# Kernel tuning notes

Measured on AMD Instinct MI355X. Metric: run time of the kernel, lower is better.

Reference implementation:

```python
import jax, jax.numpy as jnp
import numpy as np

B, S, H, NH, SPAN = 1, 2048, 768, 12, 512
D = H // NH
EPS = 1e-7
SCALE_FACTOR = 3  # 1 + len([c2p, p2c]) per DeBERTa


def setup_inputs() -> dict:
    key = jax.random.key(0)
    ks = jax.random.split(key, 10)
    r = lambda i, shape, s=0.02: jax.random.normal(ks[i], shape, jnp.float32) * s
    return dict(
        hidden_states=jax.random.normal(ks[0], (B, S, H), jnp.float32),
        attention_mask=jnp.ones((B, S), jnp.int32),
        Wq=r(1, (H, H)), bq=jnp.zeros((H,), jnp.float32),
        Wk=r(2, (H, H)), bk=jnp.zeros((H,), jnp.float32),
        Wv=r(3, (H, H)), bv=jnp.zeros((H,), jnp.float32),
        rel_embeddings=r(4, (2 * SPAN, H), 1.0),
        Wpk=r(5, (H, H)),
        Wpq=r(6, (H, H)), bpq=jnp.zeros((H,), jnp.float32),
        Wo=r(7, (H, H)), bo=jnp.zeros((H,), jnp.float32),
        ln_gamma=jnp.ones((H,), jnp.float32),
        ln_beta=jnp.zeros((H,), jnp.float32),
    )


def _heads(x):
    # [B,S,H] -> [B,NH,S,D]
    return x.reshape(B, S, NH, D).transpose(0, 2, 1, 3)


def reference(hidden_states, attention_mask, Wq, bq, Wk, bk, Wv, bv,
              rel_embeddings, Wpk, Wpq, bpq, Wo, bo, ln_gamma, ln_beta):
    q = _heads(hidden_states @ Wq + bq)
    k = _heads(hidden_states @ Wk + bk)
    v = _heads(hidden_states @ Wv + bv)
    scale = 1.0 / jnp.sqrt(jnp.asarray(D * SCALE_FACTOR, jnp.float32))

    # content-to-content
    scores = jnp.einsum('bhid,bhjd->bhij', q, k) * scale

    # relative positions: rel[i,j] = i - j
    ids = jnp.arange(S)
    rel = ids[:, None] - ids[None, :]                       # [S,S]

    pos_k = (rel_embeddings @ Wpk).reshape(2 * SPAN, NH, D)        # [2L,h,d]
    pos_q = (rel_embeddings @ Wpq + bpq).reshape(2 * SPAN, NH, D)  # [2L,h,d]

    # content-to-position: gather over clamped relative index
    c2p = jnp.einsum('bhid,lhd->bhil', q, pos_k) * scale    # [B,h,S,2L]
    c2p_idx = jnp.clip(rel + SPAN, 0, 2 * SPAN - 1)         # [S,S]
    c2p_att = c2p[:, :, ids[:, None], c2p_idx]              # [B,h,S,S]

    # position-to-content: gather then transpose (DeBERTa)
    p2c = jnp.einsum('bhjd,lhd->bhjl', k, pos_q) * scale    # [B,h,S,2L]
    p2c_idx = jnp.clip(-rel + SPAN, 0, 2 * SPAN - 1)        # [S,S]
    p2c_att = jnp.swapaxes(p2c[:, :, ids[:, None], p2c_idx], -1, -2)

    scores = scores + c2p_att + p2c_att

    mask4 = (attention_mask[:, None, None, :] * attention_mask[:, None, :, None]).astype(bool)
    scores = jnp.where(mask4, scores, jnp.finfo(scores.dtype).min)
    probs = jax.nn.softmax(scores, axis=-1)

    ctx = jnp.einsum('bhij,bhjd->bhid', probs, v).transpose(0, 2, 1, 3).reshape(B, S, H)

    # BertSelfOutput: dense + (dropout=identity) + residual + LayerNorm
    out = ctx @ Wo + bo + hidden_states
    mu = out.mean(-1, keepdims=True)
    var = out.var(-1, keepdims=True)
    return (out - mu) / jnp.sqrt(var + EPS) * ln_gamma + ln_beta
```

## Files before the change

### kernel.cpp

```cpp
#include <hip/hip_runtime.h>
#include <hip/hip_bf16.h>


typedef short v8s __attribute__((ext_vector_type(8)));
typedef short v4s __attribute__((ext_vector_type(4)));
typedef float v4f __attribute__((ext_vector_type(4)));

__device__ __forceinline__ float b2f(unsigned short u) {
    union { unsigned int i; float f; } v; v.i = ((unsigned int)u) << 16; return v.f;
}
__device__ __forceinline__ unsigned short f2b(float f) {
    union { float f; unsigned int i; } v; v.f = f;
    unsigned int x = v.i;
    return (unsigned short)((x + 0x7FFFu + ((x >> 16) & 1u)) >> 16);
}

#define SEQ 2048
#define HD  768
#define NH_ 12
#define DH  64

__global__ void cvt_kernel(const float* __restrict__ hs, const float* __restrict__ rel,
                           const float* __restrict__ bq, const float* __restrict__ bk,
                           const float* __restrict__ bv, const float* __restrict__ bpq,
                           unsigned short* __restrict__ Xb, unsigned short* __restrict__ Rb,
                           float* __restrict__ bias3, float* __restrict__ bias2) {
    long i = (long)blockIdx.x * 256 + threadIdx.x;
    const long n1 = (long)SEQ * HD;
    const long n2 = 1024l * HD;
    if (i < n1) Xb[i] = f2b(hs[i]);
    else if (i < n1 + n2) Rb[i - n1] = f2b(rel[i - n1]);
    else {
        int j = (int)(i - n1 - n2);
        if (j < 768)        bias3[j] = bq[j];
        else if (j < 1536)  bias3[j] = bk[j - 768];
        else if (j < 2304)  bias3[j] = bv[j - 1536];
        else if (j < 3072)  bias2[j - 2304] = 0.0f;
        else if (j < 3840)  bias2[j - 2304] = bpq[j - 3072];
    }
}

struct WtArgs { const float* src[6]; unsigned short* dst[6]; };
__global__ void wtrans_kernel(WtArgs args) {
    __shared__ float tile[32][33];
    const int z = blockIdx.z;
    const float* Sp = args.src[z];
    unsigned short* Dp = args.dst[z];
    const int bx = blockIdx.x * 32, by = blockIdx.y * 32;
    const int tx = threadIdx.x, ty = threadIdx.y;
#pragma unroll
    for (int r = 0; r < 32; r += 8) tile[ty + r][tx] = Sp[(by + ty + r) * HD + bx + tx];
    __syncthreads();
#pragma unroll
    for (int r = 0; r < 32; r += 8) Dp[(bx + ty + r) * HD + by + tx] = f2b(tile[tx][ty + r]);
}

__global__ void vtrans_kernel(const unsigned short* __restrict__ src,
                              unsigned short* __restrict__ dst) {
    __shared__ unsigned short tile[32][33];
    const int bx = blockIdx.x * 32, by = blockIdx.y * 32;
    const int tx = threadIdx.x, ty = threadIdx.y;
#pragma unroll
    for (int r = 0; r < 32; r += 8) tile[ty + r][tx] = src[(long)(by + ty + r) * HD + bx + tx];
    __syncthreads();
#pragma unroll
    for (int r = 0; r < 32; r += 8) dst[(long)(bx + ty + r) * SEQ + by + tx] = tile[tx][ty + r];
}

template <int BIAS, int RESID, int OUTF32>
__global__ __launch_bounds__(256) void gemm_bt(
    const unsigned short* __restrict__ A, int lda, long aBatch,
    const unsigned short* __restrict__ Bt, int ldb, long bBatch,
    void* __restrict__ Cv, int ldc, long cBatch,
    const float* __restrict__ bias, long biasBatch,
    const float* __restrict__ resid, int K) {
    __shared__ unsigned short As[128 * 72];
    __shared__ unsigned short Bs[128 * 72];
    const int z = blockIdx.z;
    const unsigned short* Ab = A + (long)z * aBatch;
    const unsigned short* Bb = Bt + (long)z * bBatch;
    const int m0 = blockIdx.y * 128, n0 = blockIdx.x * 128;
    const int t = threadIdx.x;
    const int wave = t >> 6, lane = t & 63, quad = lane >> 4, l16 = lane & 15;
    const int wm = (wave >> 1) * 64, wn = (wave & 1) * 64;
    v4f acc[4][4];
    const v4f z4 = {0.f, 0.f, 0.f, 0.f};
#pragma unroll
    for (int i = 0; i < 4; i++)
#pragma unroll
        for (int j = 0; j < 4; j++) acc[i][j] = z4;

    const int srow = t >> 1, scol = (t & 1) * 32;
    const unsigned short* ga = Ab + (long)(m0 + srow) * lda + scol;
    const unsigned short* gb = Bb + (long)(n0 + srow) * ldb + scol;
    unsigned short* wa = &As[srow * 72 + scol];
    unsigned short* wb = &Bs[srow * 72 + scol];

    for (int k0 = 0; k0 < K; k0 += 64) {
        __syncthreads();
        v8s a0 = *(const v8s*)(ga + k0);
        v8s a1 = *(const v8s*)(ga + k0 + 8);
        v8s a2 = *(const v8s*)(ga + k0 + 16);
        v8s a3 = *(const v8s*)(ga + k0 + 24);
        v8s b0 = *(const v8s*)(gb + k0);
        v8s b1 = *(const v8s*)(gb + k0 + 8);
        v8s b2 = *(const v8s*)(gb + k0 + 16);
        v8s b3 = *(const v8s*)(gb + k0 + 24);
        *(v8s*)(wa) = a0; *(v8s*)(wa + 8) = a1; *(v8s*)(wa + 16) = a2; *(v8s*)(wa + 24) = a3;
        *(v8s*)(wb) = b0; *(v8s*)(wb + 8) = b1; *(v8s*)(wb + 16) = b2; *(v8s*)(wb + 24) = b3;
        __syncthreads();
#pragma unroll
        for (int ks = 0; ks < 2; ks++) {
            v8s af[4], bf[4];
#pragma unroll
            for (int mt = 0; mt < 4; mt++)
                af[mt] = *(const v8s*)&As[(wm + 16 * mt + l16) * 72 + ks * 32 + quad * 8];
#pragma unroll
            for (int nt = 0; nt < 4; nt++)
                bf[nt] = *(const v8s*)&Bs[(wn + 16 * nt + l16) * 72 + ks * 32 + quad * 8];
#pragma unroll
            for (int mt = 0; mt < 4; mt++)
#pragma unroll
                for (int nt = 0; nt < 4; nt++)
                    acc[mt][nt] = __builtin_amdgcn_mfma_f32_16x16x32_bf16(af[mt], bf[nt], acc[mt][nt], 0, 0, 0);
        }
    }
    float* Cf = (float*)Cv;
    unsigned short* Ch = (unsigned short*)Cv;
    const long cb = (long)z * cBatch;
#pragma unroll
    for (int mt = 0; mt < 4; mt++) {
#pragma unroll
        for (int nt = 0; nt < 4; nt++) {
            const int gn = n0 + wn + 16 * nt + l16;
            float bv_ = 0.0f;
            if (BIAS) bv_ = bias[(long)z * biasBatch + gn];
#pragma unroll
            for (int r = 0; r < 4; r++) {
                const int gm = m0 + wm + 16 * mt + quad * 4 + r;
                float v = acc[mt][nt][r];
                if (BIAS) v += bv_;
                if (RESID) v += resid[(long)gm * ldc + gn];
                if (OUTF32) Cf[cb + (long)gm * ldc + gn] = v;
                else        Ch[cb + (long)gm * ldc + gn] = f2b(v);
            }
        }
    }
}

__device__ __forceinline__ void stage_window(const unsigned short* __restrict__ row,
                                             int D0, v8s& w0, v8s& w1) {
    if (D0 <= 0) {
        unsigned short v = row[0];
#pragma unroll
        for (int u = 0; u < 8; u++) { w0[u] = (short)v; w1[u] = (short)v; }
    } else if (D0 - 15 >= 1023) {
        unsigned short v = row[1023];
#pragma unroll
        for (int u = 0; u < 8; u++) { w0[u] = (short)v; w1[u] = (short)v; }
    } else if (D0 <= 1023 && D0 - 15 >= 0) {
        v8s x = *(const v8s*)(row + D0 - 7);
        v8s y = *(const v8s*)(row + D0 - 15);
#pragma unroll
        for (int u = 0; u < 8; u++) { w0[u] = x[7 - u]; w1[u] = y[7 - u]; }
    } else {
#pragma unroll
        for (int u = 0; u < 16; u++) {
            int d = D0 - u; d = d < 0 ? 0 : (d > 1023 ? 1023 : d);
            short v = (short)row[d];
            if (u < 8) w0[u] = v; else w1[u - 8] = v;
        }
    }
}

__global__ __launch_bounds__(256, 3) void flash_kernel(
    const unsigned short* __restrict__ qb, const unsigned short* __restrict__ kb,
    const unsigned short* __restrict__ vT, const unsigned short* __restrict__ c2p,
    const unsigned short* __restrict__ p2c, float* __restrict__ opart,
    float* __restrict__ mlpart) {
    __shared__ unsigned short Kl[64 * 72];
    __shared__ unsigned short Vl[64 * 72];
    __shared__ unsigned short Pl[4][16 * 72];
    __shared__ unsigned short Cw[64 * 72];
    __shared__ unsigned short Pw[64 * 72];
    const int h = blockIdx.y;
    const int i0 = blockIdx.x * 64;
    const int jc = blockIdx.z;
    const int jbase = jc * 1024;
    const int t = threadIdx.x;
    const int wave = t >> 6, lane = t & 63, quad = lane >> 4, l16 = lane & 15;
    const float scale = 0.07216878364870322f;

    v8s qf[2];
    {
        const int irow = i0 + wave * 16 + l16;
        const unsigned short* qp = qb + (long)irow * HD + h * DH + quad * 8;
        qf[0] = *(const v8s*)qp;
        qf[1] = *(const v8s*)(qp + 32);
    }
    float m_run[4] = {-1e30f, -1e30f, -1e30f, -1e30f};
    float l_run[4] = {0.f, 0.f, 0.f, 0.f};
    v4f o_acc[4];
    const v4f z4 = {0.f, 0.f, 0.f, 0.f};
#pragma unroll
    for (int nt = 0; nt < 4; nt++) o_acc[nt] = z4;

    const int srow = t >> 2, scoff = (t & 3) * 16;
    const unsigned short* kbase = kb + (long)srow * HD + h * DH + scoff;
    const unsigned short* vbase = vT + (long)(h * DH + srow) * SEQ + scoff + jbase;
    unsigned short* wk = &Kl[srow * 72 + scoff];
    unsigned short* wv = &Vl[srow * 72 + scoff];
    const unsigned short* c2prow = c2p + ((long)h * SEQ + i0 + srow) * 1024;
    const unsigned short* p2cb = p2c + (long)h * SEQ * 1024;

    v8s k0v, k1v, v0v, v1v, cw0, cw1, pw0, pw1;
    auto load_tile = [&](int j0) {
        k0v = *(const v8s*)(kbase + (long)(jbase + j0) * HD);
        k1v = *(const v8s*)(kbase + (long)(jbase + j0) * HD + 8);
        v0v = *(const v8s*)(vbase + j0);
        v1v = *(const v8s*)(vbase + j0 + 8);
        stage_window(c2prow, (i0 + srow) - (jbase + j0) - scoff + 512, cw0, cw1);
        stage_window(p2cb + (long)(jbase + j0 + srow) * 1024,
                     (jbase + j0 + srow) - i0 - scoff + 512, pw0, pw1);
    };
    load_tile(0);

    for (int tt = 0; tt < 16; tt++) {
        __syncthreads();
        *(v8s*)wk = k0v; *(v8s*)(wk + 8) = k1v;
        *(v8s*)wv = v0v; *(v8s*)(wv + 8) = v1v;
        *(v8s*)&Cw[srow * 72 + scoff] = cw0; *(v8s*)&Cw[srow * 72 + scoff + 8] = cw1;
        *(v8s*)&Pw[srow * 72 + scoff] = pw0; *(v8s*)&Pw[srow * 72 + scoff + 8] = pw1;
        if (tt + 1 < 16) load_tile((tt + 1) * 64);
        __syncthreads();

        v4f s[4];
#pragma unroll
        for (int nt = 0; nt < 4; nt++) s[nt] = z4;
#pragma unroll
        for (int ks = 0; ks < 2; ks++) {
#pragma unroll
            for (int nt = 0; nt < 4; nt++) {
                v8s bf = *(const v8s*)&Kl[(16 * nt + l16) * 72 + ks * 32 + quad * 8];
                s[nt] = __builtin_amdgcn_mfma_f32_16x16x32_bf16(qf[ks], bf, s[nt], 0, 0, 0);
            }
        }
        float sm[4][4];
#pragma unroll
        for (int nt = 0; nt < 4; nt++) {
            v4s p4 = *(const v4s*)&Pw[(nt * 16 + l16) * 72 + wave * 16 + quad * 4];
#pragma unroll
            for (int r = 0; r < 4; r++) {
                float c2pv = b2f(Cw[(wave * 16 + quad * 4 + r) * 72 + nt * 16 + l16]);
                float p2cv = b2f((unsigned short)p4[r]);
                sm[nt][r] = (s[nt][r] + c2pv + p2cv) * scale;
            }
        }
#pragma unroll
        for (int r = 0; r < 4; r++) {
            float mx = fmaxf(fmaxf(sm[0][r], sm[1][r]), fmaxf(sm[2][r], sm[3][r]));
#pragma unroll
            for (int off = 1; off < 16; off <<= 1) mx = fmaxf(mx, __shfl_xor(mx, off));
            float mnew = fmaxf(m_run[r], mx);
            float alpha = __expf(m_run[r] - mnew);
            m_run[r] = mnew;
            float rs = 0.f;
#pragma unroll
            for (int nt = 0; nt < 4; nt++) {
                float p = __expf(sm[nt][r] - mnew);
                sm[nt][r] = p;
                rs += p;
            }
#pragma unroll
            for (int off = 1; off < 16; off <<= 1) rs += __shfl_xor(rs, off);
            l_run[r] = l_run[r] * alpha + rs;
#pragma unroll
            for (int nt = 0; nt < 4; nt++) o_acc[nt][r] *= alpha;
        }
#pragma unroll
        for (int nt = 0; nt < 4; nt++)
#pragma unroll
            for (int r = 0; r < 4; r++)
                Pl[wave][(quad * 4 + r) * 72 + nt * 16 + l16] = f2b(sm[nt][r]);
        __syncthreads();
#pragma unroll
        for (int ks = 0; ks < 2; ks++) {
            v8s pf = *(const v8s*)&Pl[wave][l16 * 72 + ks * 32 + quad * 8];
#pragma unroll
            for (int nt = 0; nt < 4; nt++) {
                v8s vf = *(const v8s*)&Vl[(16 * nt + l16) * 72 + ks * 32 + quad * 8];
                o_acc[nt] = __builtin_amdgcn_mfma_f32_16x16x32_bf16(pf, vf, o_acc[nt], 0, 0, 0);
            }
        }
    }
    float* op = opart + (long)jc * SEQ * HD;
#pragma unroll
    for (int nt = 0; nt < 4; nt++) {
        const int d = nt * 16 + l16;
#pragma unroll
        for (int r = 0; r < 4; r++) {
            const int i = i0 + wave * 16 + quad * 4 + r;
            op[(long)i * HD + h * DH + d] = o_acc[nt][r];
        }
    }
    if (l16 == 0) {
#pragma unroll
        for (int r = 0; r < 4; r++) {
            const int i = i0 + wave * 16 + quad * 4 + r;
            float* ml = mlpart + (((long)jc * NH_ + h) * SEQ + i) * 2;
            ml[0] = m_run[r];
            ml[1] = l_run[r];
        }
    }
}

__global__ __launch_bounds__(256) void combine_kernel(const float* __restrict__ opart,
                                                      const float* __restrict__ mlpart,
                                                      unsigned short* __restrict__ ctx) {
    const long idx = (long)blockIdx.x * 256 + threadIdx.x;
    const int i = (int)(idx / HD);
    const int hd = (int)(idx % HD);
    const int h = hd >> 6;
    const float* ml0 = mlpart + (((long)0 * NH_ + h) * SEQ + i) * 2;
    const float* ml1 = mlpart + (((long)1 * NH_ + h) * SEQ + i) * 2;
    float m0 = ml0[0], l0 = ml0[1], m1 = ml1[0], l1 = ml1[1];
    float mM = fmaxf(m0, m1);
    float w0 = __expf(m0 - mM), w1 = __expf(m1 - mM);
    float num = w0 * opart[idx] + w1 * opart[(long)SEQ * HD + idx];
    float den = w0 * l0 + w1 * l1;
    ctx[idx] = f2b(num / den);
}

__global__ __launch_bounds__(256) void ln_kernel(const float* __restrict__ x,
                                                 const float* __restrict__ gamma,
                                                 const float* __restrict__ beta,
                                                 float* __restrict__ out) {
    const int row = blockIdx.x;
    const int t = threadIdx.x;
    const float* xr = x + (long)row * HD;
    float v0 = xr[t], v1 = xr[t + 256], v2 = xr[t + 512];
    float s = v0 + v1 + v2;
    float ss = v0 * v0 + v1 * v1 + v2 * v2;
#pragma unroll
    for (int off = 1; off < 64; off <<= 1) { s += __shfl_xor(s, off); ss += __shfl_xor(ss, off); }
    __shared__ float red[8];
    const int wave = t >> 6;
    if ((t & 63) == 0) { red[wave] = s; red[wave + 4] = ss; }
    __syncthreads();
    float S = red[0] + red[1] + red[2] + red[3];
    float SS = red[4] + red[5] + red[6] + red[7];
    const float inv = 1.0f / 768.0f;
    float mu = S * inv;
    float var = SS * inv - mu * mu;
    float rstd = rsqrtf(var + 1e-7f);
    float* orow = out + (long)row * HD;
    orow[t]       = (v0 - mu) * rstd * gamma[t]       + beta[t];
    orow[t + 256] = (v1 - mu) * rstd * gamma[t + 256] + beta[t + 256];
    orow[t + 512] = (v2 - mu) * rstd * gamma[t + 512] + beta[t + 512];
}

extern "C" void kernel_launch(void* const* d_in, const int* in_sizes, int n_in,
                              void* d_out, int out_size, void* d_ws, size_t ws_size,
                              hipStream_t stream) {
    const float* hidden = (const float*)d_in[0];
    const float* Wq  = (const float*)d_in[2];
    const float* bq  = (const float*)d_in[3];
    const float* Wk  = (const float*)d_in[4];
    const float* bk  = (const float*)d_in[5];
    const float* Wv  = (const float*)d_in[6];
    const float* bv  = (const float*)d_in[7];
    const float* rel = (const float*)d_in[8];
    const float* Wpk = (const float*)d_in[9];
    const float* Wpq = (const float*)d_in[10];
    const float* bpq = (const float*)d_in[11];
    const float* Wo  = (const float*)d_in[12];
    const float* bo  = (const float*)d_in[13];
    const float* gamma = (const float*)d_in[14];
    const float* beta  = (const float*)d_in[15];

    char* ws = (char*)d_ws;
    size_t off = 0;
    auto alloc = [&](size_t bytes) -> char* { char* p = ws + off; off += bytes; return p; };
    unsigned short* Xb   = (unsigned short*)alloc(2048ul * 768 * 2);
    unsigned short* Rb   = (unsigned short*)alloc(1024ul * 768 * 2);
    unsigned short* W3T  = (unsigned short*)alloc(3ul * 768 * 768 * 2);
    unsigned short* WoT  = (unsigned short*)alloc(768ul * 768 * 2);
    unsigned short* Wp2T = (unsigned short*)alloc(2ul * 768 * 768 * 2);
    float*          bias3 = (float*)alloc(2304 * 4);
    float*          bias2 = (float*)alloc(1536 * 4);
    unsigned short* qkv  = (unsigned short*)alloc(3ul * 2048 * 768 * 2);
    unsigned short* vTs  = (unsigned short*)alloc(768ul * 2048 * 2);
    unsigned short* pos2 = (unsigned short*)alloc(2ul * 1024 * 768 * 2);
    unsigned short* c2p  = (unsigned short*)alloc(12ul * 2048 * 1024 * 2);
    unsigned short* p2c  = (unsigned short*)alloc(12ul * 2048 * 1024 * 2);
    unsigned short* ctx  = (unsigned short*)alloc(2048ul * 768 * 2);
    float*          out_pre = (float*)alloc(2048ul * 768 * 4);
    float*          opart   = (float*)alloc(2ul * 2048 * 768 * 4);
    float*          mlpart  = (float*)alloc(2ul * 12 * 2048 * 2 * 4);
    (void)ws_size;

    cvt_kernel<<<9231, 256, 0, stream>>>(hidden, rel, bq, bk, bv, bpq, Xb, Rb, bias3, bias2);
    WtArgs wa;
    wa.src[0] = Wq;  wa.dst[0] = W3T;
    wa.src[1] = Wk;  wa.dst[1] = W3T + 768 * 768;
    wa.src[2] = Wv;  wa.dst[2] = W3T + 2 * 768 * 768;
    wa.src[3] = Wo;  wa.dst[3] = WoT;
    wa.src[4] = Wpk; wa.dst[4] = Wp2T;
    wa.src[5] = Wpq; wa.dst[5] = Wp2T + 768 * 768;
    wtrans_kernel<<<dim3(24, 24, 6), dim3(32, 8), 0, stream>>>(wa);

    gemm_bt<1, 0, 0><<<dim3(6, 16, 3), 256, 0, stream>>>(
        Xb, 768, 0, W3T, 768, 768l * 768, qkv, 768, 2048l * 768, bias3, 768, nullptr, 768);
    gemm_bt<1, 0, 0><<<dim3(6, 8, 2), 256, 0, stream>>>(
        Rb, 768, 0, Wp2T, 768, 768l * 768, pos2, 768, 1024l * 768, bias2, 768, nullptr, 768);
    vtrans_kernel<<<dim3(24, 64), dim3(32, 8), 0, stream>>>(qkv + 2ul * 2048 * 768, vTs);
    gemm_bt<0, 0, 0><<<dim3(8, 16, 12), 256, 0, stream>>>(
        qkv, 768, 64, pos2, 768, 64, c2p, 1024, 2048l * 1024, nullptr, 0, nullptr, 64);
    gemm_bt<0, 0, 0><<<dim3(8, 16, 12), 256, 0, stream>>>(
        qkv + 2048ul * 768, 768, 64, pos2 + 1024ul * 768, 768, 64, p2c, 1024, 2048l * 1024,
        nullptr, 0, nullptr, 64);
    flash_kernel<<<dim3(32, 12, 2), 256, 0, stream>>>(qkv, qkv + 2048ul * 768, vTs, c2p, p2c,
                                                      opart, mlpart);
    combine_kernel<<<6144, 256, 0, stream>>>(opart, mlpart, ctx);
    gemm_bt<1, 1, 1><<<dim3(6, 16, 1), 256, 0, stream>>>(
        ctx, 768, 0, WoT, 768, 0, out_pre, 768, 0, bo, 0, hidden, 768);
    ln_kernel<<<2048, 256, 0, stream>>>(out_pre, gamma, beta, (float*)d_out);
}
```

Measured before the change: 269.6 us.

## Fuse c2p/p2c position GEMMs into flash attention kernel, drop score buffers

Stops materialising the full c2p and p2c score tables (12x2048x1024 bf16 each) through two separate GEMM launches. The flash kernel now computes the needed 64-wide relative-position windows on the fly with MFMA against pos_k/pos_q, keeping them in small LDS rings indexed by the diagonal offset. K and V tiles are read straight from global memory instead of being staged through LDS. This removes large HBM writes and reads and two launches, at the cost of extra MFMA work and uncoalesced, unprefetched global loads inside the attention loop.

```diff
diff --git a/kernel.cpp b/kernel.cpp
--- a/kernel.cpp
+++ b/kernel.cpp
@@ -3,7 +3,6 @@
 
 
 typedef short v8s __attribute__((ext_vector_type(8)));
-typedef short v4s __attribute__((ext_vector_type(4)));
 typedef float v4f __attribute__((ext_vector_type(4)));
 
 __device__ __forceinline__ float b2f(unsigned short u) {
@@ -148,111 +147,125 @@
     }
 }
 
-__device__ __forceinline__ void stage_window(const unsigned short* __restrict__ row,
-                                             int D0, v8s& w0, v8s& w1) {
-    if (D0 <= 0) {
-        unsigned short v = row[0];
-#pragma unroll
-        for (int u = 0; u < 8; u++) { w0[u] = (short)v; w1[u] = (short)v; }
-    } else if (D0 - 15 >= 1023) {
-        unsigned short v = row[1023];
-#pragma unroll
-        for (int u = 0; u < 8; u++) { w0[u] = (short)v; w1[u] = (short)v; }
-    } else if (D0 <= 1023 && D0 - 15 >= 0) {
-        v8s x = *(const v8s*)(row + D0 - 7);
-        v8s y = *(const v8s*)(row + D0 - 15);
-#pragma unroll
-        for (int u = 0; u < 8; u++) { w0[u] = x[7 - u]; w1[u] = y[7 - u]; }
-    } else {
-#pragma unroll
-        for (int u = 0; u < 16; u++) {
-            int d = D0 - u; d = d < 0 ? 0 : (d > 1023 ? 1023 : d);
-            short v = (short)row[d];
-            if (u < 8) w0[u] = v; else w1[u - 8] = v;
-        }
-    }
-}
-
 __global__ __launch_bounds__(256, 3) void flash_kernel(
     const unsigned short* __restrict__ qb, const unsigned short* __restrict__ kb,
-    const unsigned short* __restrict__ vT, const unsigned short* __restrict__ c2p,
-    const unsigned short* __restrict__ p2c, float* __restrict__ opart,
+    const unsigned short* __restrict__ vT, const unsigned short* __restrict__ posk,
+    const unsigned short* __restrict__ posq, float* __restrict__ opart,
     float* __restrict__ mlpart) {
-    __shared__ unsigned short Kl[64 * 72];
-    __shared__ unsigned short Vl[64 * 72];
+    __shared__ unsigned short Cring[4][2][16 * 68];
+    __shared__ unsigned short Pring[2][64 * 68];
     __shared__ unsigned short Pl[4][16 * 72];
-    __shared__ unsigned short Cw[64 * 72];
-    __shared__ unsigned short Pw[64 * 72];
     const int h = blockIdx.y;
     const int i0 = blockIdx.x * 64;
-    const int jc = blockIdx.z;
-    const int jbase = jc * 1024;
+    const int jbase = blockIdx.z * 1024;
     const int t = threadIdx.x;
     const int wave = t >> 6, lane = t & 63, quad = lane >> 4, l16 = lane & 15;
     const float scale = 0.07216878364870322f;
+    const v4f z4 = {0.f, 0.f, 0.f, 0.f};
+
+    const unsigned short* pkh = posk + h * DH;
+    const unsigned short* pqh = posq + h * DH;
+    const unsigned short* kbh = kb + h * DH;
+    const unsigned short* vth = vT + (long)h * DH * SEQ;
 
     v8s qf[2];
     {
-        const int irow = i0 + wave * 16 + l16;
-        const unsigned short* qp = qb + (long)irow * HD + h * DH + quad * 8;
+        const unsigned short* qp = qb + (long)(i0 + wave * 16 + l16) * HD + h * DH + quad * 8;
         qf[0] = *(const v8s*)qp;
         qf[1] = *(const v8s*)(qp + 32);
     }
+
     float m_run[4] = {-1e30f, -1e30f, -1e30f, -1e30f};
     float l_run[4] = {0.f, 0.f, 0.f, 0.f};
     v4f o_acc[4];
-    const v4f z4 = {0.f, 0.f, 0.f, 0.f};
 #pragma unroll
     for (int nt = 0; nt < 4; nt++) o_acc[nt] = z4;
 
-    const int srow = t >> 2, scoff = (t & 3) * 16;
-    const unsigned short* kbase = kb + (long)srow * HD + h * DH + scoff;
-    const unsigned short* vbase = vT + (long)(h * DH + srow) * SEQ + scoff + jbase;
-    unsigned short* wk = &Kl[srow * 72 + scoff];
-    unsigned short* wv = &Vl[srow * 72 + scoff];
-    const unsigned short* c2prow = c2p + ((long)h * SEQ + i0 + srow) * 1024;
-    const unsigned short* p2cb = p2c + (long)h * SEQ * 1024;
-
-    v8s k0v, k1v, v0v, v1v, cw0, cw1, pw0, pw1;
-    auto load_tile = [&](int j0) {
-        k0v = *(const v8s*)(kbase + (long)(jbase + j0) * HD);
-        k1v = *(const v8s*)(kbase + (long)(jbase + j0) * HD + 8);
-        v0v = *(const v8s*)(vbase + j0);
-        v1v = *(const v8s*)(vbase + j0 + 8);
-        stage_window(c2prow, (i0 + srow) - (jbase + j0) - scoff + 512, cw0, cw1);
-        stage_window(p2cb + (long)(jbase + j0 + srow) * 1024,
-                     (jbase + j0 + srow) - i0 - scoff + 512, pw0, pw1);
+    unsigned short* cw = &Cring[wave][0][0];
+
+    auto c2p_block = [&](int b) {
+        v4f c[4] = {z4, z4, z4, z4};
+        int rr[4];
+#pragma unroll
+        for (int nt = 0; nt < 4; nt++) {
+            int r = 64 * b + 16 * nt + l16;
+            rr[nt] = r < 0 ? 0 : (r > 1023 ? 1023 : r);
+        }
+#pragma unroll
+        for (int ks = 0; ks < 2; ks++)
+#pragma unroll
+            for (int nt = 0; nt < 4; nt++) {
+                v8s bf = *(const v8s*)(pkh + (long)rr[nt] * HD + ks * 32 + quad * 8);
+                c[nt] = __builtin_amdgcn_mfma_f32_16x16x32_bf16(qf[ks], bf, c[nt], 0, 0, 0);
+            }
+        unsigned short* dst = cw + (b & 1) * (16 * 68);
+#pragma unroll
+        for (int nt = 0; nt < 4; nt++)
+#pragma unroll
+            for (int r = 0; r < 4; r++)
+                dst[(quad * 4 + r) * 68 + 16 * nt + l16] = f2b(c[nt][r]);
     };
-    load_tile(0);
 
     for (int tt = 0; tt < 16; tt++) {
+        const int j0 = jbase + 64 * tt;
+        const int D = i0 - j0 + 512;
+        const int BLc = (D >> 6) - 1;
+        const int Bp = ((j0 - i0 + 512) >> 6) - 1;
+
         __syncthreads();
-        *(v8s*)wk = k0v; *(v8s*)(wk + 8) = k1v;
-        *(v8s*)wv = v0v; *(v8s*)(wv + 8) = v1v;
-        *(v8s*)&Cw[srow * 72 + scoff] = cw0; *(v8s*)&Cw[srow * 72 + scoff + 8] = cw1;
-        *(v8s*)&Pw[srow * 72 + scoff] = pw0; *(v8s*)&Pw[srow * 72 + scoff + 8] = pw1;
-        if (tt + 1 < 16) load_tile((tt + 1) * 64);
+        if (tt == 0) c2p_block(BLc + 1);
+        c2p_block(BLc);
+        {
+            v8s af[2];
+#pragma unroll
+            for (int ks = 0; ks < 2; ks++)
+                af[ks] = *(const v8s*)(kbh + (long)(j0 + wave * 16 + l16) * HD + ks * 32 + quad * 8);
+#pragma unroll
+            for (int sel = 0; sel < 2; sel++) {
+                const int b = Bp + sel;
+                v4f p[4] = {z4, z4, z4, z4};
+                int rr[4];
+#pragma unroll
+                for (int nt = 0; nt < 4; nt++) {
+                    int r = 64 * b + 16 * nt + l16;
+                    rr[nt] = r < 0 ? 0 : (r > 1023 ? 1023 : r);
+                }
+#pragma unroll
+                for (int ks = 0; ks < 2; ks++)
+#pragma unroll
+                    for (int nt = 0; nt < 4; nt++) {
+                        v8s bf = *(const v8s*)(pqh + (long)rr[nt] * HD + ks * 32 + quad * 8);
+                        p[nt] = __builtin_amdgcn_mfma_f32_16x16x32_bf16(af[ks], bf, p[nt], 0, 0, 0);
+                    }
+#pragma unroll
+                for (int nt = 0; nt < 4; nt++)
+#pragma unroll
+                    for (int r = 0; r < 4; r++)
+                        Pring[sel][(wave * 16 + quad * 4 + r) * 68 + 16 * nt + l16] = f2b(p[nt][r]);
+            }
+        }
+        v4f s[4] = {z4, z4, z4, z4};
+#pragma unroll
+        for (int ks = 0; ks < 2; ks++)
+#pragma unroll
+            for (int nt = 0; nt < 4; nt++) {
+                v8s bf = *(const v8s*)(kbh + (long)(j0 + 16 * nt + l16) * HD + ks * 32 + quad * 8);
+                s[nt] = __builtin_amdgcn_mfma_f32_16x16x32_bf16(qf[ks], bf, s[nt], 0, 0, 0);
+            }
         __syncthreads();
 
-        v4f s[4];
-#pragma unroll
-        for (int nt = 0; nt < 4; nt++) s[nt] = z4;
-#pragma unroll
-        for (int ks = 0; ks < 2; ks++) {
-#pragma unroll
-            for (int nt = 0; nt < 4; nt++) {
-                v8s bf = *(const v8s*)&Kl[(16 * nt + l16) * 72 + ks * 32 + quad * 8];
-                s[nt] = __builtin_amdgcn_mfma_f32_16x16x32_bf16(qf[ks], bf, s[nt], 0, 0, 0);
-            }
-        }
         float sm[4][4];
 #pragma unroll
         for (int nt = 0; nt < 4; nt++) {
-            v4s p4 = *(const v4s*)&Pw[(nt * 16 + l16) * 72 + wave * 16 + quad * 4];
 #pragma unroll
             for (int r = 0; r < 4; r++) {
-                float c2pv = b2f(Cw[(wave * 16 + quad * 4 + r) * 72 + nt * 16 + l16]);
-                float p2cv = b2f((unsigned short)p4[r]);
+                const int il = wave * 16 + quad * 4 + r;
+                const int jl = nt * 16 + l16;
+                const int idx = 64 + il - jl;
+                float c2pv = b2f(cw[((BLc + (idx >> 6)) & 1) * (16 * 68) +
+                                    (quad * 4 + r) * 68 + (idx & 63)]);
+                const int idq = 128 - idx;
+                float p2cv = b2f(Pring[idq >> 6][jl * 68 + (idq & 63)]);
                 sm[nt][r] = (s[nt][r] + c2pv + p2cv) * scale;
             }
         }
@@ -288,11 +301,12 @@
             v8s pf = *(const v8s*)&Pl[wave][l16 * 72 + ks * 32 + quad * 8];
 #pragma unroll
             for (int nt = 0; nt < 4; nt++) {
-                v8s vf = *(const v8s*)&Vl[(16 * nt + l16) * 72 + ks * 32 + quad * 8];
+                v8s vf = *(const v8s*)(vth + (long)(16 * nt + l16) * SEQ + j0 + ks * 32 + quad * 8);
                 o_acc[nt] = __builtin_amdgcn_mfma_f32_16x16x32_bf16(pf, vf, o_acc[nt], 0, 0, 0);
             }
         }
     }
+    const int jc = blockIdx.z;
     float* op = opart + (long)jc * SEQ * HD;
 #pragma unroll
     for (int nt = 0; nt < 4; nt++) {
@@ -391,8 +405,6 @@
     unsigned short* qkv  = (unsigned short*)alloc(3ul * 2048 * 768 * 2);
     unsigned short* vTs  = (unsigned short*)alloc(768ul * 2048 * 2);
     unsigned short* pos2 = (unsigned short*)alloc(2ul * 1024 * 768 * 2);
-    unsigned short* c2p  = (unsigned short*)alloc(12ul * 2048 * 1024 * 2);
-    unsigned short* p2c  = (unsigned short*)alloc(12ul * 2048 * 1024 * 2);
     unsigned short* ctx  = (unsigned short*)alloc(2048ul * 768 * 2);
     float*          out_pre = (float*)alloc(2048ul * 768 * 4);
     float*          opart   = (float*)alloc(2ul * 2048 * 768 * 4);
@@ -414,13 +426,8 @@
     gemm_bt<1, 0, 0><<<dim3(6, 8, 2), 256, 0, stream>>>(
         Rb, 768, 0, Wp2T, 768, 768l * 768, pos2, 768, 1024l * 768, bias2, 768, nullptr, 768);
     vtrans_kernel<<<dim3(24, 64), dim3(32, 8), 0, stream>>>(qkv + 2ul * 2048 * 768, vTs);
-    gemm_bt<0, 0, 0><<<dim3(8, 16, 12), 256, 0, stream>>>(
-        qkv, 768, 64, pos2, 768, 64, c2p, 1024, 2048l * 1024, nullptr, 0, nullptr, 64);
-    gemm_bt<0, 0, 0><<<dim3(8, 16, 12), 256, 0, stream>>>(
-        qkv + 2048ul * 768, 768, 64, pos2 + 1024ul * 768, 768, 64, p2c, 1024, 2048l * 1024,
-        nullptr, 0, nullptr, 64);
-    flash_kernel<<<dim3(32, 12, 2), 256, 0, stream>>>(qkv, qkv + 2048ul * 768, vTs, c2p, p2c,
-                                                      opart, mlpart);
+    flash_kernel<<<dim3(32, 12, 2), 256, 0, stream>>>(qkv, qkv + 2048ul * 768, vTs,
+                                                      pos2, pos2 + 1024ul * 768, opart, mlpart);
     combine_kernel<<<6144, 256, 0, stream>>>(opart, mlpart, ctx);
     gemm_bt<1, 1, 1><<<dim3(6, 16, 1), 256, 0, stream>>>(
         ctx, 768, 0, WoT, 768, 0, out_pre, 768, 0, bo, 0, hidden, 768);
```

New measurement: 372.2 us. 1.38x slower.

## Merge prep and GEMM launches, shrink flash LDS to raise occupancy

Applied to the files above, without the earlier changes.

Folds the conversion and weight-transpose kernels into one launch, merges the QKV and positional GEMMs into one grid, and merges the c2p and p2c GEMMs into one grid, cutting the number of kernel launches and the idle gaps between them. In the flash kernel, the per-wave probability buffer now shares one LDS array with the c2p window, and the block barrier before the PV product is replaced by an LDS waitcnt. This lowers LDS use so the launch bound can ask for 4 blocks per CU instead of 3. The shared buffer relies on each wave touching only its own rows, and the strided prep loop adds some per-element overhead.

```diff
diff --git a/kernel.cpp b/kernel.cpp
--- a/kernel.cpp
+++ b/kernel.cpp
@@ -20,39 +20,44 @@
 #define NH_ 12
 #define DH  64
 
-__global__ void cvt_kernel(const float* __restrict__ hs, const float* __restrict__ rel,
-                           const float* __restrict__ bq, const float* __restrict__ bk,
-                           const float* __restrict__ bv, const float* __restrict__ bpq,
-                           unsigned short* __restrict__ Xb, unsigned short* __restrict__ Rb,
-                           float* __restrict__ bias3, float* __restrict__ bias2) {
-    long i = (long)blockIdx.x * 256 + threadIdx.x;
-    const long n1 = (long)SEQ * HD;
-    const long n2 = 1024l * HD;
-    if (i < n1) Xb[i] = f2b(hs[i]);
-    else if (i < n1 + n2) Rb[i - n1] = f2b(rel[i - n1]);
-    else {
-        int j = (int)(i - n1 - n2);
-        if (j < 768)        bias3[j] = bq[j];
-        else if (j < 1536)  bias3[j] = bk[j - 768];
-        else if (j < 2304)  bias3[j] = bv[j - 1536];
-        else if (j < 3072)  bias2[j - 2304] = 0.0f;
-        else if (j < 3840)  bias2[j - 2304] = bpq[j - 3072];
-    }
-}
-
 struct WtArgs { const float* src[6]; unsigned short* dst[6]; };
-__global__ void wtrans_kernel(WtArgs args) {
-    __shared__ float tile[32][33];
+__global__ void prep_kernel(WtArgs args, const float* __restrict__ hs,
+                            const float* __restrict__ rel,
+                            const float* __restrict__ bq, const float* __restrict__ bk,
+                            const float* __restrict__ bv, const float* __restrict__ bpq,
+                            unsigned short* __restrict__ Xb, unsigned short* __restrict__ Rb,
+                            float* __restrict__ bias3, float* __restrict__ bias2) {
     const int z = blockIdx.z;
-    const float* Sp = args.src[z];
-    unsigned short* Dp = args.dst[z];
-    const int bx = blockIdx.x * 32, by = blockIdx.y * 32;
     const int tx = threadIdx.x, ty = threadIdx.y;
-#pragma unroll
-    for (int r = 0; r < 32; r += 8) tile[ty + r][tx] = Sp[(by + ty + r) * HD + bx + tx];
-    __syncthreads();
-#pragma unroll
-    for (int r = 0; r < 32; r += 8) Dp[(bx + ty + r) * HD + by + tx] = f2b(tile[tx][ty + r]);
+    if (z < 6) {
+        __shared__ float tile[32][33];
+        const float* Sp = args.src[z];
+        unsigned short* Dp = args.dst[z];
+        const int bx = blockIdx.x * 32, by = blockIdx.y * 32;
+#pragma unroll
+        for (int r = 0; r < 32; r += 8) tile[ty + r][tx] = Sp[(by + ty + r) * HD + bx + tx];
+        __syncthreads();
+#pragma unroll
+        for (int r = 0; r < 32; r += 8) Dp[(bx + ty + r) * HD + by + tx] = f2b(tile[tx][ty + r]);
+    } else {
+        const long n1 = (long)SEQ * HD;
+        const long n2 = 1024l * HD;
+        const long N = n1 + n2 + 3840;
+        const long stride = 24l * 24 * 256;
+        long i = ((long)blockIdx.y * 24 + blockIdx.x) * 256 + ty * 32 + tx;
+        for (; i < N; i += stride) {
+            if (i < n1) Xb[i] = f2b(hs[i]);
+            else if (i < n1 + n2) Rb[i - n1] = f2b(rel[i - n1]);
+            else {
+                int j = (int)(i - n1 - n2);
+                if (j < 768)        bias3[j] = bq[j];
+                else if (j < 1536)  bias3[j] = bk[j - 768];
+                else if (j < 2304)  bias3[j] = bv[j - 1536];
+                else if (j < 3072)  bias2[j - 2304] = 0.0f;
+                else                bias2[j - 2304] = bpq[j - 3072];
+            }
+        }
+    }
 }
 
 __global__ void vtrans_kernel(const unsigned short* __restrict__ src,
@@ -68,18 +73,12 @@
 }
 
 template <int BIAS, int RESID, int OUTF32>
-__global__ __launch_bounds__(256) void gemm_bt(
-    const unsigned short* __restrict__ A, int lda, long aBatch,
-    const unsigned short* __restrict__ Bt, int ldb, long bBatch,
-    void* __restrict__ Cv, int ldc, long cBatch,
-    const float* __restrict__ bias, long biasBatch,
-    const float* __restrict__ resid, int K) {
-    __shared__ unsigned short As[128 * 72];
-    __shared__ unsigned short Bs[128 * 72];
-    const int z = blockIdx.z;
-    const unsigned short* Ab = A + (long)z * aBatch;
-    const unsigned short* Bb = Bt + (long)z * bBatch;
-    const int m0 = blockIdx.y * 128, n0 = blockIdx.x * 128;
+__device__ __forceinline__ void gemm_core(
+    const unsigned short* __restrict__ A, int lda,
+    const unsigned short* __restrict__ Bt, int ldb,
+    void* __restrict__ Cv, int ldc,
+    const float* __restrict__ bias, const float* __restrict__ resid,
+    int K, int m0, int n0, unsigned short* As, unsigned short* Bs) {
     const int t = threadIdx.x;
     const int wave = t >> 6, lane = t & 63, quad = lane >> 4, l16 = lane & 15;
     const int wm = (wave >> 1) * 64, wn = (wave & 1) * 64;
@@ -91,8 +90,8 @@
         for (int j = 0; j < 4; j++) acc[i][j] = z4;
 
     const int srow = t >> 1, scol = (t & 1) * 32;
-    const unsigned short* ga = Ab + (long)(m0 + srow) * lda + scol;
-    const unsigned short* gb = Bb + (long)(n0 + srow) * ldb + scol;
+    const unsigned short* ga = A + (long)(m0 + srow) * lda + scol;
+    const unsigned short* gb = Bt + (long)(n0 + srow) * ldb + scol;
     unsigned short* wa = &As[srow * 72 + scol];
     unsigned short* wb = &Bs[srow * 72 + scol];
 
@@ -127,25 +126,75 @@
     }
     float* Cf = (float*)Cv;
     unsigned short* Ch = (unsigned short*)Cv;
-    const long cb = (long)z * cBatch;
 #pragma unroll
     for (int mt = 0; mt < 4; mt++) {
 #pragma unroll
         for (int nt = 0; nt < 4; nt++) {
             const int gn = n0 + wn + 16 * nt + l16;
             float bv_ = 0.0f;
-            if (BIAS) bv_ = bias[(long)z * biasBatch + gn];
+            if (BIAS) bv_ = bias[gn];
 #pragma unroll
             for (int r = 0; r < 4; r++) {
                 const int gm = m0 + wm + 16 * mt + quad * 4 + r;
                 float v = acc[mt][nt][r];
                 if (BIAS) v += bv_;
                 if (RESID) v += resid[(long)gm * ldc + gn];
-                if (OUTF32) Cf[cb + (long)gm * ldc + gn] = v;
-                else        Ch[cb + (long)gm * ldc + gn] = f2b(v);
-            }
-        }
-    }
+                if (OUTF32) Cf[(long)gm * ldc + gn] = v;
+                else        Ch[(long)gm * ldc + gn] = f2b(v);
+            }
+        }
+    }
+}
+
+__global__ __launch_bounds__(256) void gemm_qkvpos(
+    const unsigned short* __restrict__ Xb, const unsigned short* __restrict__ Rb,
+    const unsigned short* __restrict__ W3T, const unsigned short* __restrict__ Wp2T,
+    const float* __restrict__ bias3, const float* __restrict__ bias2,
+    unsigned short* __restrict__ qkv, unsigned short* __restrict__ pos2) {
+    __shared__ unsigned short As[128 * 72];
+    __shared__ unsigned short Bs[128 * 72];
+    const int z = blockIdx.z;
+    if (z < 3) {
+        gemm_core<1, 0, 0>(Xb, 768, W3T + (long)z * 768 * 768, 768,
+                           qkv + (long)z * 2048 * 768, 768, bias3 + z * 768, nullptr,
+                           768, blockIdx.y * 128, blockIdx.x * 128, As, Bs);
+    } else {
+        if (blockIdx.y >= 8) return;
+        const int w = z - 3;
+        gemm_core<1, 0, 0>(Rb, 768, Wp2T + (long)w * 768 * 768, 768,
+                           pos2 + (long)w * 1024 * 768, 768, bias2 + w * 768, nullptr,
+                           768, blockIdx.y * 128, blockIdx.x * 128, As, Bs);
+    }
+}
+
+__global__ __launch_bounds__(256) void gemm_band(
+    const unsigned short* __restrict__ qkv, const unsigned short* __restrict__ pos2,
+    unsigned short* __restrict__ c2p, unsigned short* __restrict__ p2c) {
+    __shared__ unsigned short As[128 * 72];
+    __shared__ unsigned short Bs[128 * 72];
+    const int z = blockIdx.z;
+    const unsigned short* A;
+    const unsigned short* B;
+    unsigned short* C;
+    if (z < 12) {
+        A = qkv + z * 64; B = pos2 + z * 64; C = c2p + (long)z * 2048 * 1024;
+    } else {
+        const int h = z - 12;
+        A = qkv + 2048l * 768 + h * 64; B = pos2 + 1024l * 768 + h * 64;
+        C = p2c + (long)h * 2048 * 1024;
+    }
+    gemm_core<0, 0, 0>(A, 768, B, 768, C, 1024, nullptr, nullptr,
+                       64, blockIdx.y * 128, blockIdx.x * 128, As, Bs);
+}
+
+__global__ __launch_bounds__(256) void gemm_out(
+    const unsigned short* __restrict__ ctx, const unsigned short* __restrict__ WoT,
+    const float* __restrict__ bo, const float* __restrict__ hidden,
+    float* __restrict__ out_pre) {
+    __shared__ unsigned short As[128 * 72];
+    __shared__ unsigned short Bs[128 * 72];
+    gemm_core<1, 1, 1>(ctx, 768, WoT, 768, out_pre, 768, bo, hidden,
+                       768, blockIdx.y * 128, blockIdx.x * 128, As, Bs);
 }
 
 __device__ __forceinline__ void stage_window(const unsigned short* __restrict__ row,
@@ -173,16 +222,15 @@
     }
 }
 
-__global__ __launch_bounds__(256, 3) void flash_kernel(
+__global__ __launch_bounds__(256, 4) void flash_kernel(
     const unsigned short* __restrict__ qb, const unsigned short* __restrict__ kb,
     const unsigned short* __restrict__ vT, const unsigned short* __restrict__ c2p,
     const unsigned short* __restrict__ p2c, float* __restrict__ opart,
     float* __restrict__ mlpart) {
     __shared__ unsigned short Kl[64 * 72];
     __shared__ unsigned short Vl[64 * 72];
-    __shared__ unsigned short Pl[4][16 * 72];
-    __shared__ unsigned short Cw[64 * 72];
     __shared__ unsigned short Pw[64 * 72];
+    __shared__ unsigned short CwPl[64 * 72];
     const int h = blockIdx.y;
     const int i0 = blockIdx.x * 64;
     const int jc = blockIdx.z;
@@ -190,18 +238,17 @@
     const int t = threadIdx.x;
     const int wave = t >> 6, lane = t & 63, quad = lane >> 4, l16 = lane & 15;
     const float scale = 0.07216878364870322f;
+    const v4f z4 = {0.f, 0.f, 0.f, 0.f};
 
     v8s qf[2];
     {
-        const int irow = i0 + wave * 16 + l16;
-        const unsigned short* qp = qb + (long)irow * HD + h * DH + quad * 8;
+        const unsigned short* qp = qb + (long)(i0 + wave * 16 + l16) * HD + h * DH + quad * 8;
         qf[0] = *(const v8s*)qp;
         qf[1] = *(const v8s*)(qp + 32);
     }
     float m_run[4] = {-1e30f, -1e30f, -1e30f, -1e30f};
     float l_run[4] = {0.f, 0.f, 0.f, 0.f};
     v4f o_acc[4];
-    const v4f z4 = {0.f, 0.f, 0.f, 0.f};
 #pragma unroll
     for (int nt = 0; nt < 4; nt++) o_acc[nt] = z4;
 
@@ -210,18 +257,20 @@
     const unsigned short* vbase = vT + (long)(h * DH + srow) * SEQ + scoff + jbase;
     unsigned short* wk = &Kl[srow * 72 + scoff];
     unsigned short* wv = &Vl[srow * 72 + scoff];
+    unsigned short* wc = &CwPl[srow * 72 + scoff];
+    unsigned short* wp = &Pw[srow * 72 + scoff];
     const unsigned short* c2prow = c2p + ((long)h * SEQ + i0 + srow) * 1024;
     const unsigned short* p2cb = p2c + (long)h * SEQ * 1024;
 
     v8s k0v, k1v, v0v, v1v, cw0, cw1, pw0, pw1;
-    auto load_tile = [&](int j0) {
-        k0v = *(const v8s*)(kbase + (long)(jbase + j0) * HD);
-        k1v = *(const v8s*)(kbase + (long)(jbase + j0) * HD + 8);
-        v0v = *(const v8s*)(vbase + j0);
-        v1v = *(const v8s*)(vbase + j0 + 8);
-        stage_window(c2prow, (i0 + srow) - (jbase + j0) - scoff + 512, cw0, cw1);
-        stage_window(p2cb + (long)(jbase + j0 + srow) * 1024,
-                     (jbase + j0 + srow) - i0 - scoff + 512, pw0, pw1);
+    auto load_tile = [&](int j0l) {
+        k0v = *(const v8s*)(kbase + (long)(jbase + j0l) * HD);
+        k1v = *(const v8s*)(kbase + (long)(jbase + j0l) * HD + 8);
+        v0v = *(const v8s*)(vbase + j0l);
+        v1v = *(const v8s*)(vbase + j0l + 8);
+        stage_window(c2prow, (i0 + srow) - (jbase + j0l) - scoff + 512, cw0, cw1);
+        stage_window(p2cb + (long)(jbase + j0l + srow) * 1024,
+                     (jbase + j0l + srow) - i0 - scoff + 512, pw0, pw1);
     };
     load_tile(0);
 
@@ -229,31 +278,27 @@
         __syncthreads();
         *(v8s*)wk = k0v; *(v8s*)(wk + 8) = k1v;
         *(v8s*)wv = v0v; *(v8s*)(wv + 8) = v1v;
-        *(v8s*)&Cw[srow * 72 + scoff] = cw0; *(v8s*)&Cw[srow * 72 + scoff + 8] = cw1;
-        *(v8s*)&Pw[srow * 72 + scoff] = pw0; *(v8s*)&Pw[srow * 72 + scoff + 8] = pw1;
+        *(v8s*)wc = cw0; *(v8s*)(wc + 8) = cw1;
+        *(v8s*)wp = pw0; *(v8s*)(wp + 8) = pw1;
         if (tt + 1 < 16) load_tile((tt + 1) * 64);
         __syncthreads();
 
-        v4f s[4];
-#pragma unroll
-        for (int nt = 0; nt < 4; nt++) s[nt] = z4;
-#pragma unroll
-        for (int ks = 0; ks < 2; ks++) {
+        v4f s[4] = {z4, z4, z4, z4};
+#pragma unroll
+        for (int ks = 0; ks < 2; ks++)
 #pragma unroll
             for (int nt = 0; nt < 4; nt++) {
                 v8s bf = *(const v8s*)&Kl[(16 * nt + l16) * 72 + ks * 32 + quad * 8];
                 s[nt] = __builtin_amdgcn_mfma_f32_16x16x32_bf16(qf[ks], bf, s[nt], 0, 0, 0);
             }
-        }
         float sm[4][4];
 #pragma unroll
         for (int nt = 0; nt < 4; nt++) {
             v4s p4 = *(const v4s*)&Pw[(nt * 16 + l16) * 72 + wave * 16 + quad * 4];
 #pragma unroll
             for (int r = 0; r < 4; r++) {
-                float c2pv = b2f(Cw[(wave * 16 + quad * 4 + r) * 72 + nt * 16 + l16]);
-                float p2cv = b2f((unsigned short)p4[r]);
-                sm[nt][r] = (s[nt][r] + c2pv + p2cv) * scale;
+                float c2pv = b2f(CwPl[(wave * 16 + quad * 4 + r) * 72 + nt * 16 + l16]);
+                sm[nt][r] = (s[nt][r] + c2pv + b2f((unsigned short)p4[r])) * scale;
             }
         }
 #pragma unroll
@@ -281,11 +326,11 @@
         for (int nt = 0; nt < 4; nt++)
 #pragma unroll
             for (int r = 0; r < 4; r++)
-                Pl[wave][(quad * 4 + r) * 72 + nt * 16 + l16] = f2b(sm[nt][r]);
-        __syncthreads();
+                CwPl[(wave * 16 + quad * 4 + r) * 72 + nt * 16 + l16] = f2b(sm[nt][r]);
+        asm volatile("s_waitcnt lgkmcnt(0)" ::: "memory");
 #pragma unroll
         for (int ks = 0; ks < 2; ks++) {
-            v8s pf = *(const v8s*)&Pl[wave][l16 * 72 + ks * 32 + quad * 8];
+            v8s pf = *(const v8s*)&CwPl[(wave * 16 + l16) * 72 + ks * 32 + quad * 8];
 #pragma unroll
             for (int nt = 0; nt < 4; nt++) {
                 v8s vf = *(const v8s*)&Vl[(16 * nt + l16) * 72 + ks * 32 + quad * 8];
@@ -399,7 +444,6 @@
     float*          mlpart  = (float*)alloc(2ul * 12 * 2048 * 2 * 4);
     (void)ws_size;
 
-    cvt_kernel<<<9231, 256, 0, stream>>>(hidden, rel, bq, bk, bv, bpq, Xb, Rb, bias3, bias2);
     WtArgs wa;
     wa.src[0] = Wq;  wa.dst[0] = W3T;
     wa.src[1] = Wk;  wa.dst[1] = W3T + 768 * 768;
@@ -407,22 +451,15 @@
     wa.src[3] = Wo;  wa.dst[3] = WoT;
     wa.src[4] = Wpk; wa.dst[4] = Wp2T;
     wa.src[5] = Wpq; wa.dst[5] = Wp2T + 768 * 768;
-    wtrans_kernel<<<dim3(24, 24, 6), dim3(32, 8), 0, stream>>>(wa);
-
-    gemm_bt<1, 0, 0><<<dim3(6, 16, 3), 256, 0, stream>>>(
-        Xb, 768, 0, W3T, 768, 768l * 768, qkv, 768, 2048l * 768, bias3, 768, nullptr, 768);
-    gemm_bt<1, 0, 0><<<dim3(6, 8, 2), 256, 0, stream>>>(
-        Rb, 768, 0, Wp2T, 768, 768l * 768, pos2, 768, 1024l * 768, bias2, 768, nullptr, 768);
+    prep_kernel<<<dim3(24, 24, 7), dim3(32, 8), 0, stream>>>(
+        wa, hidden, rel, bq, bk, bv, bpq, Xb, Rb, bias3, bias2);
+
+    gemm_qkvpos<<<dim3(6, 16, 5), 256, 0, stream>>>(Xb, Rb, W3T, Wp2T, bias3, bias2, qkv, pos2);
     vtrans_kernel<<<dim3(24, 64), dim3(32, 8), 0, stream>>>(qkv + 2ul * 2048 * 768, vTs);
-    gemm_bt<0, 0, 0><<<dim3(8, 16, 12), 256, 0, stream>>>(
-        qkv, 768, 64, pos2, 768, 64, c2p, 1024, 2048l * 1024, nullptr, 0, nullptr, 64);
-    gemm_bt<0, 0, 0><<<dim3(8, 16, 12), 256, 0, stream>>>(
-        qkv + 2048ul * 768, 768, 64, pos2 + 1024ul * 768, 768, 64, p2c, 1024, 2048l * 1024,
-        nullptr, 0, nullptr, 64);
+    gemm_band<<<dim3(8, 16, 24), 256, 0, stream>>>(qkv, pos2, c2p, p2c);
     flash_kernel<<<dim3(32, 12, 2), 256, 0, stream>>>(qkv, qkv + 2048ul * 768, vTs, c2p, p2c,
                                                       opart, mlpart);
     combine_kernel<<<6144, 256, 0, stream>>>(opart, mlpart, ctx);
-    gemm_bt<1, 1, 1><<<dim3(6, 16, 1), 256, 0, stream>>>(
-        ctx, 768, 0, WoT, 768, 0, out_pre, 768, 0, bo, 0, hidden, 768);
+    gemm_out<<<dim3(6, 16, 1), 256, 0, stream>>>(ctx, WoT, bo, hidden, out_pre);
     ln_kernel<<<2048, 256, 0, stream>>>(out_pre, gamma, beta, (float*)d_out);
 }
```

Result: faster. 255.9 us (-5.1%).
